# Optimization experiments

Measured on AMD Instinct MI355X. Metric: run time of the kernel, lower is better.

The kernel has to match this reference:

```python
import jax, jax.numpy as jnp
import numpy as np
import math

B = 16384
INPUT = 2048
HIDDEN = 2048
PROJ = 1024


def setup_inputs() -> dict:
    key = jax.random.key(0)
    ks = jax.random.split(key, 20)
    stdv = 1.0 / math.sqrt(PROJ)
    u = lambda k, shape: jax.random.uniform(k, shape, jnp.float32, -stdv, stdv)
    return {
        "x_t": jax.random.normal(ks[0], (B, INPUT), jnp.float32),
        "h_t": jax.random.normal(ks[1], (B, PROJ), jnp.float32),
        "c_t": jax.random.normal(ks[2], (B, HIDDEN), jnp.float32),
        "weight_if_x": u(ks[3], (INPUT, 2 * HIDDEN)),
        "weight_if_h": u(ks[4], (PROJ, 2 * HIDDEN)),
        "weight_if_c": u(ks[5], (HIDDEN, 2 * HIDDEN)),
        "bias_i": u(ks[6], (HIDDEN,)),
        "bias_f": u(ks[7], (HIDDEN,)),
        "weight_c_x": u(ks[8], (INPUT, HIDDEN)),
        "weight_c_h": u(ks[9], (PROJ, HIDDEN)),
        "bias_c": u(ks[10], (HIDDEN,)),
        "weight_o_x": u(ks[11], (INPUT, PROJ)),
        "weight_o_h": u(ks[12], (PROJ, PROJ)),
        "weight_o_c": u(ks[13], (HIDDEN, PROJ)),
        "bias_o": u(ks[14], (PROJ,)),
        "weight_r_proj": u(ks[15], (HIDDEN, PROJ)),
        "weight_r_x": u(ks[16], (INPUT, PROJ)),
    }


def reference(x_t, h_t, c_t, weight_if_x, weight_if_h, weight_if_c, bias_i, bias_f,
              weight_c_x, weight_c_h, bias_c, weight_o_x, weight_o_h, weight_o_c,
              bias_o, weight_r_proj, weight_r_x):
    # input/forget gates with peephole on c_t: [B, 2*HIDDEN]
    if_gates = x_t @ weight_if_x + h_t @ weight_if_h + c_t @ weight_if_c
    ingate, forgetgate = jnp.split(if_gates, 2, axis=-1)
    ingate = jax.nn.sigmoid(ingate + bias_i)
    forgetgate = jax.nn.sigmoid(forgetgate + bias_f)
    cellgate = jnp.tanh(x_t @ weight_c_x + h_t @ weight_c_h + bias_c)
    c_new = forgetgate * c_t + ingate * cellgate
    # output gate peeps at new cell state
    outgate = jax.nn.sigmoid(x_t @ weight_o_x + h_t @ weight_o_h + c_new @ weight_o_c + bias_o)
    r_t = jnp.tanh(c_new)
    m_t = r_t @ weight_r_proj
    # input_size != proj_size -> project x for the residual connection
    h_new = outgate * (m_t + x_t @ weight_r_x)
    return (h_new, c_new)
```

## Files before the change

### kernel.cpp

```cpp
#include <hip/hip_runtime.h>
#include <hip/hip_bf16.h>
#include <math.h>

typedef unsigned short u16;
typedef __bf16 bf16x8_t __attribute__((ext_vector_type(8)));
typedef float  f32x4_t  __attribute__((ext_vector_type(4)));
typedef float  f32x8_t  __attribute__((ext_vector_type(8)));
typedef u16    u16x4_t  __attribute__((ext_vector_type(4)));
typedef u16    u16x8_t  __attribute__((ext_vector_type(8)));

__device__ __forceinline__ u16 f2b(float f) {
  unsigned u = __builtin_bit_cast(unsigned, f);
  u += 0x7fffu + ((u >> 16) & 1u);
  return (u16)(u >> 16);
}
__device__ __forceinline__ float b2f(u16 h) {
  unsigned u = ((unsigned)h) << 16;
  return __builtin_bit_cast(float, u);
}
__device__ __forceinline__ float sigm_(float x) { return 1.0f / (1.0f + __expf(-x)); }
__device__ __forceinline__ float tanh_(float x) { return 1.0f - 2.0f / (__expf(2.0f * x) + 1.0f); }

__device__ __forceinline__ void gload16(const void* g, void* l) {
  __builtin_amdgcn_global_load_lds(
      (__attribute__((address_space(1))) void*)(g),
      (__attribute__((address_space(3))) void*)(l), 16, 0, 0);
}


__global__ void cvt_act_kernel(const float* __restrict__ src, u16* __restrict__ dst,
                               int C, int KT, int c0) {
  int mb = blockIdx.x, ktl = blockIdx.y, t = threadIdx.x;
  int ktg = (c0 >> 5) + ktl;
  const float* s = src + (long)(mb * 256 + t) * C + ktl * 32;
  u16* d = dst + ((long)(mb * KT + ktg)) * 8192 + t * 8;
#pragma unroll
  for (int p = 0; p < 4; ++p) {
    f32x8_t v = *(const f32x8_t*)(s + p * 8);
    u16x8_t o;
#pragma unroll
    for (int r = 0; r < 8; ++r) o[r] = f2b(v[r]);
    *(u16x8_t*)(d + p * 2048) = o;
  }
}

__global__ void cvt_wt_kernel(const float* __restrict__ src, u16* __restrict__ dst,
                              int N, int KT, int n0, int k0) {
  int bx = blockIdx.x, by = blockIdx.y, t = threadIdx.x;
  int n = bx * 256 + t;
  int nb_g = (n0 >> 8) + bx;
  int ktg = (k0 >> 5) + by;
  float tmp[32];
#pragma unroll
  for (int kk = 0; kk < 32; ++kk)
    tmp[kk] = src[(long)(by * 32 + kk) * N + n];
  u16* d = dst + ((long)(nb_g * KT + ktg)) * 8192 + t * 8;
#pragma unroll
  for (int p = 0; p < 4; ++p) {
    u16x8_t o;
#pragma unroll
    for (int r = 0; r < 8; ++r) o[r] = f2b(tmp[p * 8 + r]);
    *(u16x8_t*)(d + p * 2048) = o;
  }
}

template <int MODE>
__global__ __launch_bounds__(512, 2) void gemm256_kernel(
    const u16* __restrict__ A, const u16* __restrict__ Bt, u16* __restrict__ Cout) {
  constexpr int KT   = (MODE == 0) ? 160 : 128;
  constexpr int NCOL = (MODE == 0) ? 8192 : 2048;
  constexpr int NBN  = NCOL / 256;
  constexpr int SLOT = 16384;

  __shared__ u16 lds[3 * SLOT];

  int bid = blockIdx.x;
  int cpx = gridDim.x >> 3;
  bid = (bid & 7) * cpx + (bid >> 3);

  int mb = bid / NBN, nb = bid % NBN;
  int m0 = mb * 256, n0 = nb * 256;

  int kt0, NT;
  if (MODE == 0) { kt0 = 0; NT = (nb < 16) ? 160 : ((nb < 28) ? 96 : 64); }
  else           { kt0 = (nb < 4) ? 0 : 64; NT = 64; }

  const int tid  = threadIdx.x;
  const int lane = tid & 63;
  const int wid  = tid >> 6;
  const int wr   = wid >> 2;
  const int wc   = wid & 3;

  const int segoff = wid * 512 + lane * 8;
  const u16* baseA = A  + ((long)(mb * KT + kt0)) * 8192 + segoff;
  const u16* baseB = Bt + ((long)(nb * KT + kt0)) * 8192 + segoff;

#define STAGE_A(t, s) do { \
    gload16(baseA + (long)(t) * 8192,        &lds[(s) * SLOT + segoff]); \
    gload16(baseA + (long)(t) * 8192 + 4096, &lds[(s) * SLOT + segoff + 4096]); } while (0)
#define STAGE_B(t, s) do { \
    gload16(baseB + (long)(t) * 8192,        &lds[(s) * SLOT + 8192 + segoff]); \
    gload16(baseB + (long)(t) * 8192 + 4096, &lds[(s) * SLOT + 8192 + segoff + 4096]); } while (0)

  const int aoff = (lane >> 4) * 2048 + (wr * 128 + (lane & 15)) * 8;
  const int boff = (lane >> 4) * 2048 + (wc * 64  + (lane & 15)) * 8;

  f32x4_t acc[8][4];
#pragma unroll
  for (int m = 0; m < 8; ++m)
#pragma unroll
    for (int n = 0; n < 4; ++n) acc[m][n] = (f32x4_t){0.f, 0.f, 0.f, 0.f};

  STAGE_A(0, 0); STAGE_B(0, 0);
  STAGE_A(1, 1); STAGE_B(1, 1);
  asm volatile("s_waitcnt vmcnt(4)" ::: "memory");
  __builtin_amdgcn_s_barrier();

  int slot = 0, s2 = 2;
  for (int t = 0; t < NT; ++t) {
    const u16* sA = &lds[slot * SLOT];
    const u16* sB = sA + 8192;
    const bool pre = (t + 2 < NT);

    bf16x8_t bv[4], av[4];
#pragma unroll
    for (int n = 0; n < 4; ++n) bv[n] = *(const bf16x8_t*)&sB[boff + n * 128];
#pragma unroll
    for (int m = 0; m < 4; ++m) av[m] = *(const bf16x8_t*)&sA[aoff + m * 128];
    if (pre) STAGE_A(t + 2, s2);
    __builtin_amdgcn_s_barrier();
    asm volatile("s_waitcnt lgkmcnt(0)" ::: "memory");
    __builtin_amdgcn_sched_barrier(0);
    __builtin_amdgcn_s_setprio(1);
#pragma unroll
    for (int m = 0; m < 4; ++m)
#pragma unroll
      for (int n = 0; n < 4; ++n)
        acc[m][n] = __builtin_amdgcn_mfma_f32_16x16x32_bf16(av[m], bv[n], acc[m][n], 0, 0, 0);
    __builtin_amdgcn_s_setprio(0);
    __builtin_amdgcn_s_barrier();

#pragma unroll
    for (int m = 0; m < 4; ++m) av[m] = *(const bf16x8_t*)&sA[aoff + 512 + m * 128];
    if (pre) STAGE_B(t + 2, s2);
    __builtin_amdgcn_s_barrier();
    asm volatile("s_waitcnt lgkmcnt(0)" ::: "memory");
    __builtin_amdgcn_sched_barrier(0);
    __builtin_amdgcn_s_setprio(1);
#pragma unroll
    for (int m = 0; m < 4; ++m)
#pragma unroll
      for (int n = 0; n < 4; ++n)
        acc[m + 4][n] = __builtin_amdgcn_mfma_f32_16x16x32_bf16(av[m], bv[n], acc[m + 4][n], 0, 0, 0);
    __builtin_amdgcn_s_setprio(0);
    if (pre) asm volatile("s_waitcnt vmcnt(4)" ::: "memory");
    else     asm volatile("s_waitcnt vmcnt(0)" ::: "memory");
    __builtin_amdgcn_s_barrier();

    slot = (slot == 2) ? 0 : slot + 1;
    s2   = (s2   == 2) ? 0 : s2   + 1;
  }
#undef STAGE_A
#undef STAGE_B

  const int lr4 = (lane >> 4) * 4;
  const int lc  = lane & 15;
#pragma unroll
  for (int m = 0; m < 8; ++m) {
    int rg = m0 + wr * 128 + m * 16 + lr4;
#pragma unroll
    for (int n = 0; n < 4; ++n) {
      int cg = n0 + wc * 64 + n * 16 + lc;
#pragma unroll
      for (int r = 0; r < 4; ++r)
        Cout[(long)(rg + r) * NCOL + cg] = f2b(acc[m][n][r]);
    }
  }
}

__global__ void pass2_kernel(const u16* __restrict__ G1, const float* __restrict__ c_t,
                             const float* __restrict__ bias_i, const float* __restrict__ bias_f,
                             const float* __restrict__ bias_c,
                             float* __restrict__ c_new_out, u16* __restrict__ A2p) {
  int mb = blockIdx.x, jg = blockIdx.y, t = threadIdx.x;
  int b = mb * 256 + t;
  int j0 = jg * 32;
  const u16* row = G1 + (long)b * 8192 + j0;
  const float* cp_p = c_t + (long)b * 2048 + j0;
  float* co_p = c_new_out + (long)b * 2048 + j0;
  u16* dc = A2p + ((long)(mb * 128 + jg)) * 8192 + t * 8;
  u16* dr = dc + (long)64 * 8192;

#pragma unroll
  for (int q = 0; q < 4; ++q) {
    u16x8_t ip = *(const u16x8_t*)(row + q * 8);
    u16x8_t fp = *(const u16x8_t*)(row + 2048 + q * 8);
    u16x8_t gp = *(const u16x8_t*)(row + 4096 + q * 8);
    f32x8_t cp = *(const f32x8_t*)(cp_p + q * 8);
    f32x8_t bi = *(const f32x8_t*)(bias_i + j0 + q * 8);
    f32x8_t bf = *(const f32x8_t*)(bias_f + j0 + q * 8);
    f32x8_t bc = *(const f32x8_t*)(bias_c + j0 + q * 8);
    f32x8_t cn;
    u16x8_t cb, rb;
#pragma unroll
    for (int r = 0; r < 8; ++r) {
      float ig = sigm_(b2f(ip[r]) + bi[r]);
      float fg = sigm_(b2f(fp[r]) + bf[r]);
      float g  = tanh_(b2f(gp[r]) + bc[r]);
      float c  = fg * cp[r] + ig * g;
      cn[r] = c;
      cb[r] = f2b(c);
      rb[r] = f2b(tanh_(c));
    }
    *(f32x8_t*)(co_p + q * 8) = cn;
    *(u16x8_t*)(dc + q * 2048) = cb;
    *(u16x8_t*)(dr + q * 2048) = rb;
  }
}

__global__ void pass3_kernel(const u16* __restrict__ G1, const u16* __restrict__ G2,
                             const float* __restrict__ bias_o, float* __restrict__ h_out) {
  long i = (long)blockIdx.x * blockDim.x + threadIdx.x;
  long e = i * 8;
  int b = (int)(e >> 10);
  int j = (int)(e & 1023);
  const u16* row1 = G1 + (long)b * 8192;
  const u16* row2 = G2 + (long)b * 2048;
  u16x8_t ogp = *(const u16x8_t*)(row1 + 6144 + j);
  u16x8_t xrp = *(const u16x8_t*)(row1 + 7168 + j);
  u16x8_t ocg = *(const u16x8_t*)(row2 + j);
  u16x8_t mt  = *(const u16x8_t*)(row2 + 1024 + j);
  f32x8_t bo  = *(const f32x8_t*)(bias_o + j);
  f32x8_t h;
#pragma unroll
  for (int r = 0; r < 8; ++r) {
    float og = sigm_(b2f(ogp[r]) + b2f(ocg[r]) + bo[r]);
    h[r] = og * (b2f(mt[r]) + b2f(xrp[r]));
  }
  *(f32x8_t*)(h_out + (long)b * 1024 + j) = h;
}

extern "C" void kernel_launch(void* const* d_in, const int* in_sizes, int n_in,
                              void* d_out, int out_size, void* d_ws, size_t ws_size,
                              hipStream_t stream) {
  const float* x_t      = (const float*)d_in[0];
  const float* h_t      = (const float*)d_in[1];
  const float* c_t      = (const float*)d_in[2];
  const float* w_if_x   = (const float*)d_in[3];
  const float* w_if_h   = (const float*)d_in[4];
  const float* w_if_c   = (const float*)d_in[5];
  const float* bias_i   = (const float*)d_in[6];
  const float* bias_f   = (const float*)d_in[7];
  const float* w_c_x    = (const float*)d_in[8];
  const float* w_c_h    = (const float*)d_in[9];
  const float* bias_c   = (const float*)d_in[10];
  const float* w_o_x    = (const float*)d_in[11];
  const float* w_o_h    = (const float*)d_in[12];
  const float* w_o_c    = (const float*)d_in[13];
  const float* bias_o   = (const float*)d_in[14];
  const float* w_r_proj = (const float*)d_in[15];
  const float* w_r_x    = (const float*)d_in[16];

  char* ws = (char*)d_ws;
  u16* A1p  = (u16*)(ws);
  u16* W1tp = (u16*)(ws + 167772160L);
  u16* G1   = (u16*)(ws + 251658240L);
  u16* W2tp = (u16*)(ws + 520093696L);
  u16* A2p  = (u16*)(ws);
  u16* G2   = (u16*)(ws + 167772160L);

  float* h_out = (float*)d_out;
  float* c_out = h_out + 16384L * 1024L;

  cvt_act_kernel<<<dim3(64, 64), 256, 0, stream>>>(x_t, A1p, 2048, 160, 0);
  cvt_act_kernel<<<dim3(64, 32), 256, 0, stream>>>(h_t, A1p, 1024, 160, 2048);
  cvt_act_kernel<<<dim3(64, 64), 256, 0, stream>>>(c_t, A1p, 2048, 160, 3072);

  cvt_wt_kernel<<<dim3(16, 64), 256, 0, stream>>>(w_if_x,   W1tp, 4096, 160, 0,    0);
  cvt_wt_kernel<<<dim3(16, 32), 256, 0, stream>>>(w_if_h,   W1tp, 4096, 160, 0,    2048);
  cvt_wt_kernel<<<dim3(16, 64), 256, 0, stream>>>(w_if_c,   W1tp, 4096, 160, 0,    3072);
  cvt_wt_kernel<<<dim3(8,  64), 256, 0, stream>>>(w_c_x,    W1tp, 2048, 160, 4096, 0);
  cvt_wt_kernel<<<dim3(8,  32), 256, 0, stream>>>(w_c_h,    W1tp, 2048, 160, 4096, 2048);
  cvt_wt_kernel<<<dim3(4,  64), 256, 0, stream>>>(w_o_x,    W1tp, 1024, 160, 6144, 0);
  cvt_wt_kernel<<<dim3(4,  32), 256, 0, stream>>>(w_o_h,    W1tp, 1024, 160, 6144, 2048);
  cvt_wt_kernel<<<dim3(4,  64), 256, 0, stream>>>(w_r_x,    W1tp, 1024, 160, 7168, 0);
  cvt_wt_kernel<<<dim3(4,  64), 256, 0, stream>>>(w_o_c,    W2tp, 1024, 128, 0,    0);
  cvt_wt_kernel<<<dim3(4,  64), 256, 0, stream>>>(w_r_proj, W2tp, 1024, 128, 1024, 2048);

  gemm256_kernel<0><<<2048, 512, 0, stream>>>(A1p, W1tp, G1);

  pass2_kernel<<<dim3(64, 64), 256, 0, stream>>>(G1, c_t, bias_i, bias_f, bias_c, c_out, A2p);

  gemm256_kernel<1><<<512, 512, 0, stream>>>(A2p, W2tp, G2);

  pass3_kernel<<<8192, 256, 0, stream>>>(G1, G2, bias_o, h_out);
}
```

Baseline: 1.511 ms.

## Merge two MFMA phases per K-step and vectorize epilogue stores via operand swap

The GEMM main loop now issues both A and B prefetches for tile t+2 up front, then loads all eight A fragments and runs all 32 MFMAs in one phase, dropping the intermediate barriers and lgkmcnt waits. The MFMA operands are swapped so each lane holds four consecutive columns of one row, which lets the epilogue write four bf16 values as one 8-byte store instead of four scalar stores. This cuts barrier and synchronisation overhead and store instruction count. In exchange it raises register pressure (eight A fragments live) and removes the finer interleaving of LDS reads with compute.

```diff
diff --git a/kernel.cpp b/kernel.cpp
--- a/kernel.cpp
+++ b/kernel.cpp
@@ -122,37 +122,22 @@
     const u16* sB = sA + 8192;
     const bool pre = (t + 2 < NT);
 
-    bf16x8_t bv[4], av[4];
+    if (pre) { STAGE_A(t + 2, s2); STAGE_B(t + 2, s2); }
+
+    bf16x8_t bv[4], av[8];
 #pragma unroll
     for (int n = 0; n < 4; ++n) bv[n] = *(const bf16x8_t*)&sB[boff + n * 128];
 #pragma unroll
-    for (int m = 0; m < 4; ++m) av[m] = *(const bf16x8_t*)&sA[aoff + m * 128];
-    if (pre) STAGE_A(t + 2, s2);
-    __builtin_amdgcn_s_barrier();
-    asm volatile("s_waitcnt lgkmcnt(0)" ::: "memory");
-    __builtin_amdgcn_sched_barrier(0);
+    for (int m = 0; m < 8; ++m) av[m] = *(const bf16x8_t*)&sA[aoff + m * 128];
+
     __builtin_amdgcn_s_setprio(1);
 #pragma unroll
-    for (int m = 0; m < 4; ++m)
+    for (int m = 0; m < 8; ++m)
 #pragma unroll
       for (int n = 0; n < 4; ++n)
-        acc[m][n] = __builtin_amdgcn_mfma_f32_16x16x32_bf16(av[m], bv[n], acc[m][n], 0, 0, 0);
+        acc[m][n] = __builtin_amdgcn_mfma_f32_16x16x32_bf16(bv[n], av[m], acc[m][n], 0, 0, 0);
     __builtin_amdgcn_s_setprio(0);
-    __builtin_amdgcn_s_barrier();
-
-#pragma unroll
-    for (int m = 0; m < 4; ++m) av[m] = *(const bf16x8_t*)&sA[aoff + 512 + m * 128];
-    if (pre) STAGE_B(t + 2, s2);
-    __builtin_amdgcn_s_barrier();
-    asm volatile("s_waitcnt lgkmcnt(0)" ::: "memory");
-    __builtin_amdgcn_sched_barrier(0);
-    __builtin_amdgcn_s_setprio(1);
-#pragma unroll
-    for (int m = 0; m < 4; ++m)
-#pragma unroll
-      for (int n = 0; n < 4; ++n)
-        acc[m + 4][n] = __builtin_amdgcn_mfma_f32_16x16x32_bf16(av[m], bv[n], acc[m + 4][n], 0, 0, 0);
-    __builtin_amdgcn_s_setprio(0);
+
     if (pre) asm volatile("s_waitcnt vmcnt(4)" ::: "memory");
     else     asm volatile("s_waitcnt vmcnt(0)" ::: "memory");
     __builtin_amdgcn_s_barrier();
@@ -163,17 +148,18 @@
 #undef STAGE_A
 #undef STAGE_B
 
-  const int lr4 = (lane >> 4) * 4;
-  const int lc  = lane & 15;
+  const int rowm = lane & 15;
+  const int col4 = (lane >> 4) * 4;
 #pragma unroll
   for (int m = 0; m < 8; ++m) {
-    int rg = m0 + wr * 128 + m * 16 + lr4;
+    long rg = (long)(m0 + wr * 128 + m * 16 + rowm) * NCOL;
 #pragma unroll
     for (int n = 0; n < 4; ++n) {
-      int cg = n0 + wc * 64 + n * 16 + lc;
-#pragma unroll
-      for (int r = 0; r < 4; ++r)
-        Cout[(long)(rg + r) * NCOL + cg] = f2b(acc[m][n][r]);
+      int cg = n0 + wc * 64 + n * 16 + col4;
+      u16x4_t o;
+#pragma unroll
+      for (int r = 0; r < 4; ++r) o[r] = f2b(acc[m][n][r]);
+      *(u16x4_t*)&Cout[rg + cg] = o;
     }
   }
 }
```

After: 1.501 ms. About the same (-0.7%).
